# Kernel tuning notes

Measured on AMD Instinct MI355X. Metric: run time of the kernel, lower is better.

The kernel has to match this reference:

```python
import jax, jax.numpy as jnp
import numpy as np

B, T, D_IN = 64, 512, 512
D_HID, D_OUT = 1024, 512
NUM_DAYS = 24
EPS = 1e-5


def setup_inputs() -> dict:
    key = jax.random.key(0)
    ks = jax.random.split(key, 8)
    x = jax.random.normal(ks[0], (B, T, D_IN), dtype=jnp.float32)
    day_indices = jax.random.randint(ks[1], (B,), 0, NUM_DAYS)
    s1 = 1.0 / np.sqrt(D_IN)
    s2 = 1.0 / np.sqrt(D_HID)
    W1 = jax.random.uniform(ks[2], (NUM_DAYS, D_IN, D_HID), jnp.float32, -s1, s1)
    b1 = jax.random.uniform(ks[3], (NUM_DAYS, D_HID), jnp.float32, -s1, s1)
    W2 = jax.random.uniform(ks[4], (NUM_DAYS, D_HID, D_OUT), jnp.float32, -s2, s2)
    b2 = jax.random.uniform(ks[5], (NUM_DAYS, D_OUT), jnp.float32, -s2, s2)
    gamma = jnp.ones((NUM_DAYS, D_OUT), jnp.float32)
    beta = jnp.zeros((NUM_DAYS, D_OUT), jnp.float32)
    return {"x": x, "day_indices": day_indices, "W1": W1, "b1": b1,
            "W2": W2, "b2": b2, "gamma": gamma, "beta": beta}


def reference(x, day_indices, W1, b1, W2, b2, gamma, beta):
    # Gather each sample's day-specific adapter params, then one batched pass.
    # Equivalent to the per-day mask/gather/scatter loop in the torch module.
    # Dropout is identity (eval mode).
    W1d = W1[day_indices]                      # [B, D_in, D_hid]
    b1d = b1[day_indices][:, None, :]          # [B, 1, D_hid]
    W2d = W2[day_indices]                      # [B, D_hid, D_out]
    b2d = b2[day_indices][:, None, :]          # [B, 1, D_out]
    h = jax.nn.relu(jnp.einsum('btd,bdh->bth', x, W1d) + b1d)
    y = jnp.einsum('bth,bho->bto', h, W2d) + b2d
    # per-day LayerNorm over last dim
    mean = jnp.mean(y, axis=-1, keepdims=True)
    var = jnp.var(y, axis=-1, keepdims=True)
    y_hat = (y - mean) * jax.lax.rsqrt(var + EPS)
    g = gamma[day_indices][:, None, :]
    bt = beta[day_indices][:, None, :]
    return y_hat * g + bt
```

## Files before the change

### kernel.cpp

```cpp
#include <hip/hip_runtime.h>

#define B_    64
#define T_    512
#define DIN   512
#define DHID  1024
#define DOUT  512
#define NDAYS 24

typedef unsigned short u16;
typedef __bf16 bf16x8 __attribute__((ext_vector_type(8)));
typedef u16    u16x8  __attribute__((ext_vector_type(8)));
typedef float  f32x4  __attribute__((ext_vector_type(4)));

static __device__ __forceinline__ u16 f2bf(float f) {
    union { float f; unsigned u; } v; v.f = f;
    unsigned r = v.u + 0x7FFFu + ((v.u >> 16) & 1u);
    return (u16)(r >> 16);
}
static __device__ __forceinline__ float bf2f(u16 h) {
    union { unsigned u; float f; } v; v.u = ((unsigned)h) << 16;
    return v.f;
}

static __device__ __forceinline__ void gload_lds16(const void* g, void* l) {
    __builtin_amdgcn_global_load_lds(
        (const __attribute__((address_space(1))) void*)g,
        (__attribute__((address_space(3))) void*)l, 16, 0, 0);
}

static __device__ __forceinline__ void transpose64_body(
    const float* __restrict__ W, u16* __restrict__ WT,
    int R, int C, int j, int tid)
{
    __shared__ float t[64][65];
    const int gx = C >> 6, gy = R >> 6;
    const int bx = j % gx;
    const int by = (j / gx) % gy;
    const int d  = j / (gx * gy);
    const int r0 = by * 64, c0 = bx * 64;
    const float* Wd = W + (size_t)d * R * C;
    u16* WTd = WT + (size_t)d * R * C;

#pragma unroll
    for (int i = 0; i < 4; ++i) {
        const int row = i * 16 + (tid >> 4);
        const int col = (tid & 15) * 4;
        const float4 v = *(const float4*)&Wd[(size_t)(r0 + row) * C + c0 + col];
        t[row][col]     = v.x;
        t[row][col + 1] = v.y;
        t[row][col + 2] = v.z;
        t[row][col + 3] = v.w;
    }
    __syncthreads();
#pragma unroll
    for (int p = 0; p < 2; ++p) {
        const int c  = p * 32 + (tid >> 3);
        const int rs = (tid & 7) * 8;
        u16x8 o;
#pragma unroll
        for (int k = 0; k < 8; ++k) o[k] = f2bf(t[rs + k][c]);
        *(u16x8*)&WTd[(size_t)(c0 + c) * R + r0 + rs] = o;
    }
}

__global__ __launch_bounds__(256)
void transpose64(const float* __restrict__ W, u16* __restrict__ WT, int R, int C) {
    transpose64_body(W, WT, R, C, blockIdx.x, threadIdx.x);
}

__global__ __launch_bounds__(256)
void aux_prep(const float* __restrict__ W1, u16* __restrict__ W1T,
              const float* __restrict__ W2, u16* __restrict__ W2T,
              const float* __restrict__ x, u16* __restrict__ xb,
              int nW2)
{
    const int jb = blockIdx.x;
    const int tid = threadIdx.x;
    constexpr int NW1 = NDAYS * (DIN / 64) * (DHID / 64);
    if (jb < NW1) {
        transpose64_body(W1, W1T, DIN, DHID, jb, tid);
    } else if (jb < NW1 + nW2) {
        transpose64_body(W2, W2T, DHID, DOUT, jb - NW1, tid);
    } else {
        const int n8 = B_ * T_ * DIN / 8;
        const int ncvt = gridDim.x - NW1 - nW2;
        int i = (jb - NW1 - nW2) * 256 + tid;
        const int stride = ncvt * 256;
        for (; i < n8; i += stride) {
            float4 a = ((const float4*)x)[i * 2];
            float4 b = ((const float4*)x)[i * 2 + 1];
            u16x8 p;
            p[0] = f2bf(a.x); p[1] = f2bf(a.y); p[2] = f2bf(a.z); p[3] = f2bf(a.w);
            p[4] = f2bf(b.x); p[5] = f2bf(b.y); p[6] = f2bf(b.z); p[7] = f2bf(b.w);
            ((u16x8*)xb)[i] = p;
        }
    }
}

template<int MT, int NT, int KT, bool RELU, bool OUT_BF16>
__global__ __launch_bounds__(512, 1)
void gemm8(const u16* __restrict__ Aall,
           const u16* __restrict__ BT,
           const float* __restrict__ bias,
           const int* __restrict__ didx,
           void* __restrict__ Call)
{
    constexpr int GX = MT / 256;
    constexpr int GY = NT / 256;
    constexpr int NWG = GX * GY * B_;
    constexpr int NT_K = KT / 64;
    static_assert(NT_K >= 2 && (NWG % 8) == 0, "geometry");

    constexpr int Q = NWG / 8;
    const int hw = blockIdx.x;
    const int l  = (hw & 7) * Q + (hw >> 3);
    const int bx = l % GX;
    const int by = (l / GX) % GY;
    const int bz = l / (GX * GY);

    const int day = didx[bz];
    const int m0 = bx * 256, n0 = by * 256;
    const int tid = threadIdx.x;
    const int wv = tid >> 6, ln = tid & 63;
    const int wm = wv >> 2, wn = wv & 3;

    __shared__ __align__(16) u16 sA[2][256 * 64];
    __shared__ __align__(16) u16 sB[2][256 * 64];

    const u16* Ab = Aall + (size_t)bz * MT * KT + (size_t)m0 * KT;
    const u16* Bt = BT + (size_t)day * NT * KT + (size_t)n0 * KT;

    auto stageA = [&](int buf, int t, int h) {
#pragma unroll
        for (int c = 0; c < 2; ++c) {
            const int rl = h * 128 + wv * 16 + c * 8 + (ln >> 3);
            const int cd = (ln & 7) ^ (rl & 7);
            gload_lds16(Ab + (size_t)rl * KT + t * 64 + cd * 8,
                        (char*)&sA[buf][(h * 128 + wv * 16 + c * 8) * 64]);
        }
    };
    auto stageB = [&](int buf, int t, int h) {
#pragma unroll
        for (int c = 0; c < 2; ++c) {
            const int rl = h * 128 + wv * 16 + c * 8 + (ln >> 3);
            const int cd = (ln & 7) ^ (rl & 7);
            gload_lds16(Bt + (size_t)rl * KT + t * 64 + cd * 8,
                        (char*)&sB[buf][(h * 128 + wv * 16 + c * 8) * 64]);
        }
    };

    f32x4 acc[8][4];
#pragma unroll
    for (int i = 0; i < 8; ++i)
#pragma unroll
        for (int j = 0; j < 4; ++j)
            acc[i][j] = (f32x4){0.f, 0.f, 0.f, 0.f};

    stageA(0, 0, 0); stageB(0, 0, 0); stageA(0, 0, 1); stageB(0, 0, 1);
    stageA(1, 1, 0); stageB(1, 1, 0);
    asm volatile("s_waitcnt vmcnt(4)" ::: "memory");
    __builtin_amdgcn_s_barrier();

    for (int t = 0; t < NT_K; ++t) {
        const int buf = t & 1;
        const u16* sAb = sA[buf];
        const u16* sBb = sB[buf];
        bf16x8 av0[2][4], av1[2][4], bv0[2][2], bv1[2][2];

        auto readAv = [&](bf16x8 (&dst)[2][4], int mq) {
#pragma unroll
            for (int ks = 0; ks < 2; ++ks)
#pragma unroll
                for (int mi = 0; mi < 4; ++mi) {
                    const int r = mq * 128 + wm * 64 + mi * 16 + (ln & 15);
                    const int slot = (ks * 4 + (ln >> 4)) ^ (r & 7);
                    dst[ks][mi] = *(const bf16x8*)&sAb[r * 64 + slot * 8];
                }
        };
        auto readBv = [&](bf16x8 (&dst)[2][2], int nq) {
#pragma unroll
            for (int ks = 0; ks < 2; ++ks)
#pragma unroll
                for (int ni = 0; ni < 2; ++ni) {
                    const int r = nq * 128 + wn * 32 + ni * 16 + (ln & 15);
                    const int slot = (ks * 4 + (ln >> 4)) ^ (r & 7);
                    dst[ks][ni] = *(const bf16x8*)&sBb[r * 64 + slot * 8];
                }
        };
        auto mfmaQ = [&](bf16x8 (&a)[2][4], bf16x8 (&b)[2][2], int mq, int nq) {
#pragma unroll
            for (int ks = 0; ks < 2; ++ks)
#pragma unroll
                for (int mi = 0; mi < 4; ++mi)
#pragma unroll
                    for (int ni = 0; ni < 2; ++ni)
                        acc[mq * 4 + mi][nq * 2 + ni] =
                            __builtin_amdgcn_mfma_f32_16x16x32_bf16(
                                a[ks][mi], b[ks][ni],
                                acc[mq * 4 + mi][nq * 2 + ni], 0, 0, 0);
        };

        readAv(av0, 0); readAv(av1, 1); readBv(bv0, 0);
        if (t + 1 < NT_K) { stageA(buf ^ 1, t + 1, 1); stageB(buf ^ 1, t + 1, 1); }
        __builtin_amdgcn_s_barrier();
        asm volatile("s_waitcnt lgkmcnt(0)" ::: "memory");
        __builtin_amdgcn_sched_barrier(0);
        __builtin_amdgcn_s_setprio(1);
        mfmaQ(av0, bv0, 0, 0);
        mfmaQ(av1, bv0, 1, 0);
        __builtin_amdgcn_s_setprio(0);
        __builtin_amdgcn_s_barrier();

        readBv(bv1, 1);
        if (t + 2 < NT_K) { stageA(buf, t + 2, 0); stageB(buf, t + 2, 0); }
        __builtin_amdgcn_s_barrier();
        asm volatile("s_waitcnt lgkmcnt(0)" ::: "memory");
        __builtin_amdgcn_sched_barrier(0);
        __builtin_amdgcn_s_setprio(1);
        mfmaQ(av1, bv1, 1, 1);
        mfmaQ(av0, bv1, 0, 1);
        __builtin_amdgcn_s_setprio(0);
        if (t + 2 < NT_K) asm volatile("s_waitcnt vmcnt(4)" ::: "memory");
        else              asm volatile("s_waitcnt vmcnt(0)" ::: "memory");
        __builtin_amdgcn_s_barrier();
    }

    const float* bs = bias + (size_t)day * NT + n0;
#pragma unroll
    for (int nq = 0; nq < 2; ++nq)
#pragma unroll
        for (int ni = 0; ni < 2; ++ni) {
            const int col = nq * 128 + wn * 32 + ni * 16 + (ln & 15);
            const float bval = bs[col];
#pragma unroll
            for (int mq = 0; mq < 2; ++mq)
#pragma unroll
                for (int mi = 0; mi < 4; ++mi)
#pragma unroll
                    for (int i = 0; i < 4; ++i) {
                        const int row = mq * 128 + wm * 64 + mi * 16 + (ln >> 4) * 4 + i;
                        float v = acc[mq * 4 + mi][nq * 2 + ni][i] + bval;
                        if (RELU) v = fmaxf(v, 0.f);
                        const size_t off = (size_t)bz * MT * NT + (size_t)(m0 + row) * NT + (n0 + col);
                        if (OUT_BF16) ((u16*)Call)[off] = f2bf(v);
                        else          ((float*)Call)[off] = v;
                    }
        }
}

__global__ __launch_bounds__(512, 1)
void gemm2_ln(const u16* __restrict__ Aall,
              const u16* __restrict__ BT,
              const float* __restrict__ bias,
              const int* __restrict__ didx,
              const float* __restrict__ gamma,
              const float* __restrict__ beta,
              float* __restrict__ out)
{
    constexpr int BM = 128, BK = 64;
    constexpr int KT = DHID;
    constexpr int NT_K = KT / BK;
    constexpr int GX = T_ / BM;
    constexpr int NWG = GX * B_;

    constexpr int Q = NWG / 8;
    const int hw = blockIdx.x;
    const int l  = (hw & 7) * Q + (hw >> 3);
    const int bx = l % GX;
    const int bz = l / GX;

    const int day = didx[bz];
    const int m0 = bx * BM;
    const int tid = threadIdx.x;
    const int wv = tid >> 6, ln = tid & 63;
    const int wm = wv >> 2, wn = wv & 3;

    __shared__ __align__(16) u16 sA[2][BM * BK];
    __shared__ __align__(16) u16 sB[2][DOUT * BK];

    const u16* Ab = Aall + (size_t)bz * T_ * KT + (size_t)m0 * KT;
    const u16* Bt = BT + (size_t)day * DOUT * KT;

    auto stageA = [&](int buf, int t) {
#pragma unroll
        for (int c = 0; c < 2; ++c) {
            const int rl = wv * 16 + c * 8 + (ln >> 3);
            const int cd = (ln & 7) ^ (rl & 7);
            gload_lds16(Ab + (size_t)rl * KT + t * BK + cd * 8,
                        (char*)&sA[buf][(wv * 16 + c * 8) * BK]);
        }
    };
    auto stageBh = [&](int buf, int t, int h) {
#pragma unroll
        for (int c = 0; c < 4; ++c) {
            const int rl = h * 256 + wv * 32 + c * 8 + (ln >> 3);
            const int cd = (ln & 7) ^ (rl & 7);
            gload_lds16(Bt + (size_t)rl * KT + t * BK + cd * 8,
                        (char*)&sB[buf][(h * 256 + wv * 32 + c * 8) * BK]);
        }
    };

    f32x4 acc[4][8];
#pragma unroll
    for (int i = 0; i < 4; ++i)
#pragma unroll
        for (int j = 0; j < 8; ++j)
            acc[i][j] = (f32x4){0.f, 0.f, 0.f, 0.f};

    stageA(0, 0); stageBh(0, 0, 0); stageBh(0, 0, 1);
    stageA(1, 1); stageBh(1, 1, 0);
    asm volatile("s_waitcnt vmcnt(5)" ::: "memory");
    __builtin_amdgcn_s_barrier();

    for (int t = 0; t < NT_K; ++t) {
        const int buf = t & 1;
        const u16* sAb = sA[buf];
        const u16* sBb = sB[buf];
        bf16x8 av[2][4], bvA[2][2], bvB[2][2];

        auto readBv = [&](bf16x8 (&dst)[2][2], int nq) {
#pragma unroll
            for (int ks = 0; ks < 2; ++ks)
#pragma unroll
                for (int ni = 0; ni < 2; ++ni) {
                    const int r = nq * 128 + wn * 32 + ni * 16 + (ln & 15);
                    const int slot = (ks * 4 + (ln >> 4)) ^ (r & 7);
                    dst[ks][ni] = *(const bf16x8*)&sBb[r * BK + slot * 8];
                }
        };
        auto mfmaQ = [&](bf16x8 (&b)[2][2], int nq) {
#pragma unroll
            for (int ks = 0; ks < 2; ++ks)
#pragma unroll
                for (int mi = 0; mi < 4; ++mi)
#pragma unroll
                    for (int ni = 0; ni < 2; ++ni)
                        acc[mi][nq * 2 + ni] =
                            __builtin_amdgcn_mfma_f32_16x16x32_bf16(
                                av[ks][mi], b[ks][ni],
                                acc[mi][nq * 2 + ni], 0, 0, 0);
        };

#pragma unroll
        for (int ks = 0; ks < 2; ++ks)
#pragma unroll
            for (int mi = 0; mi < 4; ++mi) {
                const int r = wm * 64 + mi * 16 + (ln & 15);
                const int slot = (ks * 4 + (ln >> 4)) ^ (r & 7);
                av[ks][mi] = *(const bf16x8*)&sAb[r * BK + slot * 8];
            }
        readBv(bvA, 0); readBv(bvB, 1);
        if (t + 1 < NT_K) stageBh(buf ^ 1, t + 1, 1);
        __builtin_amdgcn_s_barrier();
        asm volatile("s_waitcnt lgkmcnt(0)" ::: "memory");
        __builtin_amdgcn_sched_barrier(0);
        __builtin_amdgcn_s_setprio(1);
        mfmaQ(bvA, 0);
        mfmaQ(bvB, 1);
        __builtin_amdgcn_s_setprio(0);
        __builtin_amdgcn_s_barrier();

        readBv(bvA, 2); readBv(bvB, 3);
        if (t + 2 < NT_K) { stageA(buf, t + 2); stageBh(buf, t + 2, 0); }
        __builtin_amdgcn_s_barrier();
        asm volatile("s_waitcnt lgkmcnt(0)" ::: "memory");
        __builtin_amdgcn_sched_barrier(0);
        __builtin_amdgcn_s_setprio(1);
        mfmaQ(bvA, 2);
        mfmaQ(bvB, 3);
        __builtin_amdgcn_s_setprio(0);
        if (t + 2 < NT_K) asm volatile("s_waitcnt vmcnt(5)" ::: "memory");
        else              asm volatile("s_waitcnt vmcnt(0)" ::: "memory");
        __builtin_amdgcn_s_barrier();
    }

    const float* bs = bias + (size_t)day * DOUT;
    float bval[8];
#pragma unroll
    for (int f = 0; f < 8; ++f)
        bval[f] = bs[(f >> 1) * 128 + wn * 32 + (f & 1) * 16 + (ln & 15)];

    u16* yb = (u16*)&sB[0][0];
#pragma unroll
    for (int mi = 0; mi < 4; ++mi)
#pragma unroll
        for (int f = 0; f < 8; ++f) {
            const int col = (f >> 1) * 128 + wn * 32 + (f & 1) * 16 + (ln & 15);
#pragma unroll
            for (int i = 0; i < 4; ++i) {
                const int rloc = wm * 64 + mi * 16 + (ln >> 4) * 4 + i;
                yb[rloc * DOUT + col] = f2bf(acc[mi][f][i] + bval[f]);
            }
        }
    __syncthreads();

    const float* gs = gamma + (size_t)day * DOUT;
    const float* es = beta + (size_t)day * DOUT;
    const float4 g0 = ((const float4*)gs)[ln * 2];
    const float4 g1 = ((const float4*)gs)[ln * 2 + 1];
    const float4 e0 = ((const float4*)es)[ln * 2];
    const float4 e1 = ((const float4*)es)[ln * 2 + 1];

    float* op = out + (size_t)bz * T_ * DOUT + (size_t)m0 * DOUT;
#pragma unroll 4
    for (int r = wv * 16; r < wv * 16 + 16; ++r) {
        const u16x8 yv = *(const u16x8*)&yb[r * DOUT + ln * 8];
        float yf[8];
#pragma unroll
        for (int j = 0; j < 8; ++j) yf[j] = bf2f(yv[j]);
        float s = 0.f, q = 0.f;
#pragma unroll
        for (int j = 0; j < 8; ++j) { s += yf[j]; q += yf[j] * yf[j]; }
#pragma unroll
        for (int o = 32; o; o >>= 1) { s += __shfl_xor(s, o); q += __shfl_xor(q, o); }
        const float mean = s * (1.f / 512.f);
        const float var  = q * (1.f / 512.f) - mean * mean;
        const float rstd = rsqrtf(var + 1e-5f);
        float4 o0, o1;
        o0.x = (yf[0] - mean) * rstd * g0.x + e0.x;
        o0.y = (yf[1] - mean) * rstd * g0.y + e0.y;
        o0.z = (yf[2] - mean) * rstd * g0.z + e0.z;
        o0.w = (yf[3] - mean) * rstd * g0.w + e0.w;
        o1.x = (yf[4] - mean) * rstd * g1.x + e1.x;
        o1.y = (yf[5] - mean) * rstd * g1.y + e1.y;
        o1.z = (yf[6] - mean) * rstd * g1.z + e1.z;
        o1.w = (yf[7] - mean) * rstd * g1.w + e1.w;
        ((float4*)(op + (size_t)r * DOUT))[ln * 2] = o0;
        ((float4*)(op + (size_t)r * DOUT))[ln * 2 + 1] = o1;
    }
}

extern "C" void kernel_launch(void* const* d_in, const int* in_sizes, int n_in,
                              void* d_out, int out_size, void* d_ws, size_t ws_size,
                              hipStream_t stream)
{
    const float* x     = (const float*)d_in[0];
    const int*   didx  = (const int*)d_in[1];
    const float* W1    = (const float*)d_in[2];
    const float* b1    = (const float*)d_in[3];
    const float* W2    = (const float*)d_in[4];
    const float* b2    = (const float*)d_in[5];
    const float* gamma = (const float*)d_in[6];
    const float* beta  = (const float*)d_in[7];
    float* out = (float*)d_out;

    char* ws = (char*)d_ws;
    u16* W1T = (u16*)ws;
    u16* h   = (u16*)(ws + 25165824);
    u16* xb  = (u16*)(ws + 92274688);

    const bool bigws = ws_size >= 150994944ULL;
    constexpr int NW = NDAYS * (DIN / 64) * (DHID / 64);

    if (bigws) {
        u16* W2T = (u16*)(ws + 125829120);
        aux_prep<<<NW * 2 + 2048, 256, 0, stream>>>(W1, W1T, W2, W2T, x, xb, NW);
        gemm8<T_, DHID, DIN, true, true>
            <<<dim3(2 * 4 * B_), 512, 0, stream>>>(xb, W1T, b1, didx, h);
        gemm2_ln<<<dim3(4 * B_), 512, 0, stream>>>(h, W2T, b2, didx, gamma, beta, out);
    } else {
        u16* W2T = xb;
        aux_prep<<<NW + 2048, 256, 0, stream>>>(W1, W1T, W2, W2T, x, xb, 0);
        gemm8<T_, DHID, DIN, true, true>
            <<<dim3(2 * 4 * B_), 512, 0, stream>>>(xb, W1T, b1, didx, h);
        transpose64<<<NW, 256, 0, stream>>>(W2, W2T, DHID, DOUT);
        gemm2_ln<<<dim3(4 * B_), 512, 0, stream>>>(h, W2T, b2, didx, gamma, beta, out);
    }
}
```

Baseline: 143.9 us.

## Make GEMM1 workgroups loop over both M tiles with LDS-staged coalesced stores

The first GEMM now launches half as many workgroups. Each one handles both 256-row M tiles for its (batch, N-tile) pair, prefetching the second tile's operands right after storing the first. The epilogue stages bias+ReLU bf16 results through LDS and writes them to global memory as coalesced 16-byte rows instead of scattered 2-byte stores. The aim is to cut the wave count on a 256-CU-class part so there is no partial second wave, and to improve store efficiency. The cost is serialized work per workgroup and B-tile reloads that are not reused across M tiles.

Result: slower. 210.8 us (+46.5%).

```diff
diff --git a/kernel.cpp b/kernel.cpp
--- a/kernel.cpp
+++ b/kernel.cpp
@@ -97,46 +97,43 @@
     }
 }
 
-template<int MT, int NT, int KT, bool RELU, bool OUT_BF16>
 __global__ __launch_bounds__(512, 1)
-void gemm8(const u16* __restrict__ Aall,
+void gemm1(const u16* __restrict__ Aall,
            const u16* __restrict__ BT,
            const float* __restrict__ bias,
            const int* __restrict__ didx,
-           void* __restrict__ Call)
+           u16* __restrict__ H)
 {
+    constexpr int MT = T_, NT = DHID, KT = DIN;
     constexpr int GX = MT / 256;
     constexpr int GY = NT / 256;
-    constexpr int NWG = GX * GY * B_;
+    constexpr int NWG = GY * B_;
     constexpr int NT_K = KT / 64;
-    static_assert(NT_K >= 2 && (NWG % 8) == 0, "geometry");
 
     constexpr int Q = NWG / 8;
     const int hw = blockIdx.x;
     const int l  = (hw & 7) * Q + (hw >> 3);
-    const int bx = l % GX;
-    const int by = (l / GX) % GY;
-    const int bz = l / (GX * GY);
+    const int by = l % GY;
+    const int bz = l / GY;
 
     const int day = didx[bz];
-    const int m0 = bx * 256, n0 = by * 256;
+    const int n0 = by * 256;
     const int tid = threadIdx.x;
     const int wv = tid >> 6, ln = tid & 63;
     const int wm = wv >> 2, wn = wv & 3;
 
-    __shared__ __align__(16) u16 sA[2][256 * 64];
-    __shared__ __align__(16) u16 sB[2][256 * 64];
-
-    const u16* Ab = Aall + (size_t)bz * MT * KT + (size_t)m0 * KT;
+    __shared__ __align__(16) u16 smem[4][256 * 64];
+
     const u16* Bt = BT + (size_t)day * NT * KT + (size_t)n0 * KT;
-
-    auto stageA = [&](int buf, int t, int h) {
+    const u16* Abase = Aall + (size_t)bz * MT * KT;
+
+    auto stageA = [&](const u16* Ab, int buf, int t, int h) {
 #pragma unroll
         for (int c = 0; c < 2; ++c) {
             const int rl = h * 128 + wv * 16 + c * 8 + (ln >> 3);
             const int cd = (ln & 7) ^ (rl & 7);
             gload_lds16(Ab + (size_t)rl * KT + t * 64 + cd * 8,
-                        (char*)&sA[buf][(h * 128 + wv * 16 + c * 8) * 64]);
+                        (char*)&smem[buf][(h * 128 + wv * 16 + c * 8) * 64]);
         }
     };
     auto stageB = [&](int buf, int t, int h) {
@@ -145,107 +142,137 @@
             const int rl = h * 128 + wv * 16 + c * 8 + (ln >> 3);
             const int cd = (ln & 7) ^ (rl & 7);
             gload_lds16(Bt + (size_t)rl * KT + t * 64 + cd * 8,
-                        (char*)&sB[buf][(h * 128 + wv * 16 + c * 8) * 64]);
+                        (char*)&smem[2 + buf][(h * 128 + wv * 16 + c * 8) * 64]);
         }
     };
 
-    f32x4 acc[8][4];
-#pragma unroll
-    for (int i = 0; i < 8; ++i)
-#pragma unroll
-        for (int j = 0; j < 4; ++j)
-            acc[i][j] = (f32x4){0.f, 0.f, 0.f, 0.f};
-
-    stageA(0, 0, 0); stageB(0, 0, 0); stageA(0, 0, 1); stageB(0, 0, 1);
-    stageA(1, 1, 0); stageB(1, 1, 0);
-    asm volatile("s_waitcnt vmcnt(4)" ::: "memory");
-    __builtin_amdgcn_s_barrier();
-
-    for (int t = 0; t < NT_K; ++t) {
-        const int buf = t & 1;
-        const u16* sAb = sA[buf];
-        const u16* sBb = sB[buf];
-        bf16x8 av0[2][4], av1[2][4], bv0[2][2], bv1[2][2];
-
-        auto readAv = [&](bf16x8 (&dst)[2][4], int mq) {
-#pragma unroll
-            for (int ks = 0; ks < 2; ++ks)
-#pragma unroll
-                for (int mi = 0; mi < 4; ++mi) {
-                    const int r = mq * 128 + wm * 64 + mi * 16 + (ln & 15);
-                    const int slot = (ks * 4 + (ln >> 4)) ^ (r & 7);
-                    dst[ks][mi] = *(const bf16x8*)&sAb[r * 64 + slot * 8];
-                }
-        };
-        auto readBv = [&](bf16x8 (&dst)[2][2], int nq) {
-#pragma unroll
-            for (int ks = 0; ks < 2; ++ks)
-#pragma unroll
-                for (int ni = 0; ni < 2; ++ni) {
-                    const int r = nq * 128 + wn * 32 + ni * 16 + (ln & 15);
-                    const int slot = (ks * 4 + (ln >> 4)) ^ (r & 7);
-                    dst[ks][ni] = *(const bf16x8*)&sBb[r * 64 + slot * 8];
-                }
-        };
-        auto mfmaQ = [&](bf16x8 (&a)[2][4], bf16x8 (&b)[2][2], int mq, int nq) {
-#pragma unroll
-            for (int ks = 0; ks < 2; ++ks)
-#pragma unroll
-                for (int mi = 0; mi < 4; ++mi)
-#pragma unroll
-                    for (int ni = 0; ni < 2; ++ni)
-                        acc[mq * 4 + mi][nq * 2 + ni] =
-                            __builtin_amdgcn_mfma_f32_16x16x32_bf16(
-                                a[ks][mi], b[ks][ni],
-                                acc[mq * 4 + mi][nq * 2 + ni], 0, 0, 0);
-        };
-
-        readAv(av0, 0); readAv(av1, 1); readBv(bv0, 0);
-        if (t + 1 < NT_K) { stageA(buf ^ 1, t + 1, 1); stageB(buf ^ 1, t + 1, 1); }
-        __builtin_amdgcn_s_barrier();
+    const float* bs = bias + (size_t)day * NT + n0;
+    float bval[2][2];
+#pragma unroll
+    for (int nq = 0; nq < 2; ++nq)
+#pragma unroll
+        for (int ni = 0; ni < 2; ++ni)
+            bval[nq][ni] = bs[nq * 128 + wn * 32 + ni * 16 + (ln & 15)];
+
+    {
+        const u16* Ab = Abase;
+        stageA(Ab, 0, 0, 0); stageB(0, 0, 0); stageA(Ab, 0, 0, 1); stageB(0, 0, 1);
+        stageA(Ab, 1, 1, 0); stageB(1, 1, 0);
+    }
+
+    for (int bx = 0; bx < GX; ++bx) {
+        const u16* Ab = Abase + (size_t)bx * 256 * KT;
+        const int m0 = bx * 256;
+
+        asm volatile("s_waitcnt vmcnt(4)" ::: "memory");
+        __builtin_amdgcn_s_barrier();
+
+        f32x4 acc[8][4];
+#pragma unroll
+        for (int i = 0; i < 8; ++i)
+#pragma unroll
+            for (int j = 0; j < 4; ++j)
+                acc[i][j] = (f32x4){0.f, 0.f, 0.f, 0.f};
+
+        for (int t = 0; t < NT_K; ++t) {
+            const int buf = t & 1;
+            const u16* sAb = smem[buf];
+            const u16* sBb = smem[2 + buf];
+            bf16x8 av0[2][4], av1[2][4], bv0[2][2], bv1[2][2];
+
+            auto readAv = [&](bf16x8 (&dst)[2][4], int mq) {
+#pragma unroll
+                for (int ks = 0; ks < 2; ++ks)
+#pragma unroll
+                    for (int mi = 0; mi < 4; ++mi) {
+                        const int r = mq * 128 + wm * 64 + mi * 16 + (ln & 15);
+                        const int slot = (ks * 4 + (ln >> 4)) ^ (r & 7);
+                        dst[ks][mi] = *(const bf16x8*)&sAb[r * 64 + slot * 8];
+                    }
+            };
+            auto readBv = [&](bf16x8 (&dst)[2][2], int nq) {
+#pragma unroll
+                for (int ks = 0; ks < 2; ++ks)
+#pragma unroll
+                    for (int ni = 0; ni < 2; ++ni) {
+                        const int r = nq * 128 + wn * 32 + ni * 16 + (ln & 15);
+                        const int slot = (ks * 4 + (ln >> 4)) ^ (r & 7);
+                        dst[ks][ni] = *(const bf16x8*)&sBb[r * 64 + slot * 8];
+                    }
+            };
+            auto mfmaQ = [&](bf16x8 (&a)[2][4], bf16x8 (&b)[2][2], int mq, int nq) {
+#pragma unroll
+                for (int ks = 0; ks < 2; ++ks)
+#pragma unroll
+                    for (int mi = 0; mi < 4; ++mi)
+#pragma unroll
+                        for (int ni = 0; ni < 2; ++ni)
+                            acc[mq * 4 + mi][nq * 2 + ni] =
+                                __builtin_amdgcn_mfma_f32_16x16x32_bf16(
+                                    a[ks][mi], b[ks][ni],
+                                    acc[mq * 4 + mi][nq * 2 + ni], 0, 0, 0);
+            };
+
+            readAv(av0, 0); readAv(av1, 1); readBv(bv0, 0);
+            if (t + 1 < NT_K) { stageA(Ab, buf ^ 1, t + 1, 1); stageB(buf ^ 1, t + 1, 1); }
+            __builtin_amdgcn_s_barrier();
+            asm volatile("s_waitcnt lgkmcnt(0)" ::: "memory");
+            __builtin_amdgcn_sched_barrier(0);
+            __builtin_amdgcn_s_setprio(1);
+            mfmaQ(av0, bv0, 0, 0);
+            mfmaQ(av1, bv0, 1, 0);
+            __builtin_amdgcn_s_setprio(0);
+            __builtin_amdgcn_s_barrier();
+
+            readBv(bv1, 1);
+            if (t + 2 < NT_K) { stageA(Ab, buf, t + 2, 0); stageB(buf, t + 2, 0); }
+            __builtin_amdgcn_s_barrier();
+            asm volatile("s_waitcnt lgkmcnt(0)" ::: "memory");
+            __builtin_amdgcn_sched_barrier(0);
+            __builtin_amdgcn_s_setprio(1);
+            mfmaQ(av1, bv1, 1, 1);
+            mfmaQ(av0, bv1, 0, 1);
+            __builtin_amdgcn_s_setprio(0);
+            if (t + 2 < NT_K) asm volatile("s_waitcnt vmcnt(4)" ::: "memory");
+            else              asm volatile("s_waitcnt vmcnt(0)" ::: "memory");
+            __builtin_amdgcn_s_barrier();
+        }
+
+        u16* yb = &smem[0][0];
+#pragma unroll
+        for (int mq = 0; mq < 2; ++mq)
+#pragma unroll
+            for (int mi = 0; mi < 4; ++mi)
+#pragma unroll
+                for (int nq = 0; nq < 2; ++nq)
+#pragma unroll
+                    for (int ni = 0; ni < 2; ++ni) {
+                        const int col = nq * 128 + wn * 32 + ni * 16 + (ln & 15);
+#pragma unroll
+                        for (int i = 0; i < 4; ++i) {
+                            const int row = mq * 128 + wm * 64 + mi * 16 + (ln >> 4) * 4 + i;
+                            yb[row * 256 + col] =
+                                f2bf(fmaxf(acc[mq * 4 + mi][nq * 2 + ni][i] + bval[nq][ni], 0.f));
+                        }
+                    }
+        __syncthreads();
+
+        u16* Hb = H + (size_t)bz * MT * NT + (size_t)m0 * NT + n0;
+#pragma unroll
+        for (int j = 0; j < 16; ++j) {
+            const int row = wv * 32 + j * 2 + (ln >> 5);
+            const u16x8 v = *(const u16x8*)&yb[row * 256 + (ln & 31) * 8];
+            *(u16x8*)&Hb[(size_t)row * NT + (ln & 31) * 8] = v;
+        }
         asm volatile("s_waitcnt lgkmcnt(0)" ::: "memory");
-        __builtin_amdgcn_sched_barrier(0);
-        __builtin_amdgcn_s_setprio(1);
-        mfmaQ(av0, bv0, 0, 0);
-        mfmaQ(av1, bv0, 1, 0);
-        __builtin_amdgcn_s_setprio(0);
-        __builtin_amdgcn_s_barrier();
-
-        readBv(bv1, 1);
-        if (t + 2 < NT_K) { stageA(buf, t + 2, 0); stageB(buf, t + 2, 0); }
-        __builtin_amdgcn_s_barrier();
-        asm volatile("s_waitcnt lgkmcnt(0)" ::: "memory");
-        __builtin_amdgcn_sched_barrier(0);
-        __builtin_amdgcn_s_setprio(1);
-        mfmaQ(av1, bv1, 1, 1);
-        mfmaQ(av0, bv1, 0, 1);
-        __builtin_amdgcn_s_setprio(0);
-        if (t + 2 < NT_K) asm volatile("s_waitcnt vmcnt(4)" ::: "memory");
-        else              asm volatile("s_waitcnt vmcnt(0)" ::: "memory");
-        __builtin_amdgcn_s_barrier();
-    }
-
-    const float* bs = bias + (size_t)day * NT + n0;
-#pragma unroll
-    for (int nq = 0; nq < 2; ++nq)
-#pragma unroll
-        for (int ni = 0; ni < 2; ++ni) {
-            const int col = nq * 128 + wn * 32 + ni * 16 + (ln & 15);
-            const float bval = bs[col];
-#pragma unroll
-            for (int mq = 0; mq < 2; ++mq)
-#pragma unroll
-                for (int mi = 0; mi < 4; ++mi)
-#pragma unroll
-                    for (int i = 0; i < 4; ++i) {
-                        const int row = mq * 128 + wm * 64 + mi * 16 + (ln >> 4) * 4 + i;
-                        float v = acc[mq * 4 + mi][nq * 2 + ni][i] + bval;
-                        if (RELU) v = fmaxf(v, 0.f);
-                        const size_t off = (size_t)bz * MT * NT + (size_t)(m0 + row) * NT + (n0 + col);
-                        if (OUT_BF16) ((u16*)Call)[off] = f2bf(v);
-                        else          ((float*)Call)[off] = v;
-                    }
-        }
+        __builtin_amdgcn_s_barrier();
+
+        if (bx == 0) {
+            const u16* Ab1 = Abase + (size_t)256 * KT;
+            stageA(Ab1, 0, 0, 0); stageB(0, 0, 0); stageA(Ab1, 0, 0, 1); stageB(0, 0, 1);
+            stageA(Ab1, 1, 1, 0); stageB(1, 1, 0);
+        }
+    }
 }
 
 __global__ __launch_bounds__(512, 1)
@@ -455,14 +482,12 @@
     if (bigws) {
         u16* W2T = (u16*)(ws + 125829120);
         aux_prep<<<NW * 2 + 2048, 256, 0, stream>>>(W1, W1T, W2, W2T, x, xb, NW);
-        gemm8<T_, DHID, DIN, true, true>
-            <<<dim3(2 * 4 * B_), 512, 0, stream>>>(xb, W1T, b1, didx, h);
+        gemm1<<<dim3(4 * B_), 512, 0, stream>>>(xb, W1T, b1, didx, h);
         gemm2_ln<<<dim3(4 * B_), 512, 0, stream>>>(h, W2T, b2, didx, gamma, beta, out);
     } else {
         u16* W2T = xb;
         aux_prep<<<NW + 2048, 256, 0, stream>>>(W1, W1T, W2, W2T, x, xb, 0);
-        gemm8<T_, DHID, DIN, true, true>
-            <<<dim3(2 * 4 * B_), 512, 0, stream>>>(xb, W1T, b1, didx, h);
+        gemm1<<<dim3(4 * B_), 512, 0, stream>>>(xb, W1T, b1, didx, h);
         transpose64<<<NW, 256, 0, stream>>>(W2, W2T, DHID, DOUT);
         gemm2_ln<<<dim3(4 * B_), 512, 0, stream>>>(h, W2T, b2, didx, gamma, beta, out);
     }
```
